# Kernel optimization log

Measured on AMD Instinct MI355X. Metric: run time of the kernel, lower is better.

The kernel has to match this reference:

```python
import jax, jax.numpy as jnp
import numpy as np

N_LAYERS = 3
N_HEADS = 8
N_HIDDEN = 16  # hidden_dim // n_heads
HIDDEN = 128
SLOPE = 0.2


def setup_inputs() -> dict:
    key = jax.random.key(0)
    ks = jax.random.split(key, 7)
    B, N, Din, Dh = 4, 512, 2, HIDDEN
    node_features = jax.random.normal(ks[0], (B, N, Din), dtype=jnp.float32)
    adj = jax.random.randint(ks[1], (B, N, N), 0, 2).astype(jnp.int32)
    adj = jnp.maximum(adj, jnp.eye(N, dtype=jnp.int32)[None])  # self loops -> no empty softmax rows
    s = 1.0 / np.sqrt(Dh)
    W_in = jax.random.normal(ks[2], (Din, Dh), dtype=jnp.float32) * (1.0 / np.sqrt(Din))
    W_l = jax.random.normal(ks[3], (N_LAYERS, Dh, N_HEADS * N_HIDDEN), dtype=jnp.float32) * s
    W_r = jax.random.normal(ks[4], (N_LAYERS, Dh, N_HEADS * N_HIDDEN), dtype=jnp.float32) * s
    attn_a = jax.random.normal(ks[5], (N_LAYERS, N_HIDDEN), dtype=jnp.float32) * (1.0 / np.sqrt(N_HIDDEN))
    W_out = jax.random.normal(ks[6], (Dh, 1), dtype=jnp.float32) * s
    return {"node_features": node_features, "adj": adj, "W_in": W_in,
            "W_l": W_l, "W_r": W_r, "attn_a": attn_a, "W_out": W_out}


def _gatv2_layer(h, adj, Wl, Wr, a):
    # h: [B,N,Dh]; adj: [B,N,N] int; Wl/Wr: [Dh, H*F]; a: [F]
    B, N, _ = h.shape
    g_l = (h @ Wl).reshape(B, N, N_HEADS, N_HIDDEN)
    g_r = (h @ Wr).reshape(B, N, N_HEADS, N_HIDDEN)
    # torch: g_sum[b,i,j] = g_l[b,j] + g_r[b,i]  (repeat vs repeat_interleave)
    g_sum = g_r[:, :, None, :, :] + g_l[:, None, :, :, :]  # [B,N,N,H,F]
    e = jnp.einsum('bijhf,f->bijh', jax.nn.leaky_relu(g_sum, SLOPE), a)  # [B,N,N,H]
    e = jnp.where(adj[..., None] == 0, -jnp.inf, e)
    att = jax.nn.softmax(e, axis=2)  # softmax over neighbors j
    out = jnp.einsum('bijh,bjhf->bihf', att, g_r)  # aggregate g_r (per source)
    return out.reshape(B, N, N_HEADS * N_HIDDEN)


def reference(node_features, adj, W_in, W_l, W_r, attn_a, W_out):
    h = node_features @ W_in  # [B,N,128]
    for i in range(N_LAYERS):
        h = _gatv2_layer(h, adj, W_l[i], W_r[i], attn_a[i])
    return h @ W_out  # [B,N,1]
```

## Files before the change

kernel.cpp:

```cpp
#include <hip/hip_runtime.h>
#include <cstdint>
#include <math.h>

#define NB 4
#define NN 512
#define DH 128
#define NHEADS 8
#define NHID 16
#define ITILE 64
#define SENTINEL -1e30f

__global__ __launch_bounds__(512, 1) void gat_layer(
    const int lay,
    const float* __restrict__ X, const float* __restrict__ hin,
    float* __restrict__ hout,
    const float* __restrict__ Win,
    const float* __restrict__ WlL, const float* __restrict__ WrL,
    const float* __restrict__ a_vec, const float* __restrict__ Wout,
    float* __restrict__ out, uint32_t* __restrict__ adjb,
    const int* __restrict__ adj)
{
    __shared__ __align__(16) float smem[23968];
    float* s_W   = smem;
    float* s_acc = smem + 4096;
    float* s_Win = smem + 20480;
    float* s_dgl = smem + 20736;
    float* s_dgr = smem + 21248;
    float* s_m   = smem + 21760;
    float* s_l   = smem + 22800;
    float* s_M   = smem + 23840;
    float* s_inv = smem + 23904;
    float4* Sgl  = (float4*)(smem + 4096);
    float4* Sgr  = (float4*)(smem + 12288);

    const int blk = blockIdx.x;
    const int it  = blk & 7;
    const int bh  = blk >> 3;
    const int b   = bh >> 3;
    const int hh  = bh & 7;
    const int i0  = it * ITILE;
    const int t   = threadIdx.x;
    const int il  = t & 31;
    const int js  = t >> 5;
    const int r0  = i0 + il;
    const int r1  = r0 + 32;

    {
        const int sk = t >> 2, sq = (t & 3) * 4;
        *(float4*)&s_W[sk * 32 + sq]      = *(const float4*)&WlL[sk * DH + hh * NHID + sq];
        *(float4*)&s_W[sk * 32 + 16 + sq] = *(const float4*)&WrL[sk * DH + hh * NHID + sq];
        if (lay == 0 && t < 64) ((float4*)s_Win)[t] = ((const float4*)Win)[t];
    }

    float a[16];
#pragma unroll
    for (int q = 0; q < 4; ++q) {
        const float4 v = ((const float4*)a_vec)[q];
        a[4*q+0] = v.x; a[4*q+1] = v.y; a[4*q+2] = v.z; a[4*q+3] = v.w;
    }

    uint32_t mask0, mask1;
    if (lay == 0) {
        const int4* p0 = (const int4*)(adj + ((size_t)(b * NN + r0)) * NN + js * 32);
        const int4* p1 = (const int4*)(adj + ((size_t)(b * NN + r1)) * NN + js * 32);
        uint32_t m0 = 0, m1 = 0;
#pragma unroll
        for (int c = 0; c < 8; ++c) {
            const int4 v0 = p0[c], v1 = p1[c];
            m0 |= (v0.x != 0 ? 1u : 0u) << (c * 4 + 0);
            m0 |= (v0.y != 0 ? 1u : 0u) << (c * 4 + 1);
            m0 |= (v0.z != 0 ? 1u : 0u) << (c * 4 + 2);
            m0 |= (v0.w != 0 ? 1u : 0u) << (c * 4 + 3);
            m1 |= (v1.x != 0 ? 1u : 0u) << (c * 4 + 0);
            m1 |= (v1.y != 0 ? 1u : 0u) << (c * 4 + 1);
            m1 |= (v1.z != 0 ? 1u : 0u) << (c * 4 + 2);
            m1 |= (v1.w != 0 ? 1u : 0u) << (c * 4 + 3);
        }
        mask0 = m0; mask1 = m1;
        adjb[((size_t)(b * NN + r0)) * 16 + js] = m0;
        adjb[((size_t)(b * NN + r1)) * 16 + js] = m1;
    } else {
        mask0 = adjb[((size_t)(b * NN + r0)) * 16 + js];
        mask1 = adjb[((size_t)(b * NN + r1)) * 16 + js];
    }
    __syncthreads();

    float4 agl[4], agr[4];
#pragma unroll
    for (int q = 0; q < 4; ++q) {
        agl[q].x = 0.f; agl[q].y = 0.f; agl[q].z = 0.f; agl[q].w = 0.f;
        agr[q].x = 0.f; agr[q].y = 0.f; agr[q].z = 0.f; agr[q].w = 0.f;
    }
    {
        const float* hrow = (lay > 0) ? (hin + ((size_t)(b * NN + t)) * DH) : nullptr;
        float x0 = 0.f, x1 = 0.f;
        if (lay == 0) {
            x0 = X[(b * NN + t) * 2 + 0];
            x1 = X[(b * NN + t) * 2 + 1];
        }
#pragma unroll 2
        for (int k = 0; k < DH; k += 4) {
            float4 h4;
            if (lay == 0) {
                const float4 w0 = *(const float4*)&s_Win[k];
                const float4 w1 = *(const float4*)&s_Win[DH + k];
                h4.x = x0 * w0.x + x1 * w1.x;
                h4.y = x0 * w0.y + x1 * w1.y;
                h4.z = x0 * w0.z + x1 * w1.z;
                h4.w = x0 * w0.w + x1 * w1.w;
            } else {
                h4 = *(const float4*)&hrow[k];
            }
            const float* hp = &h4.x;
#pragma unroll
            for (int kk = 0; kk < 4; ++kk) {
                const float hk = hp[kk];
                const float* wrow = &s_W[(k + kk) * 32];
#pragma unroll
                for (int q = 0; q < 4; ++q) {
                    const float4 wl = *(const float4*)&wrow[q * 4];
                    const float4 wr = *(const float4*)&wrow[16 + q * 4];
                    agl[q].x = fmaf(hk, wl.x, agl[q].x);
                    agl[q].y = fmaf(hk, wl.y, agl[q].y);
                    agl[q].z = fmaf(hk, wl.z, agl[q].z);
                    agl[q].w = fmaf(hk, wl.w, agl[q].w);
                    agr[q].x = fmaf(hk, wr.x, agr[q].x);
                    agr[q].y = fmaf(hk, wr.y, agr[q].y);
                    agr[q].z = fmaf(hk, wr.z, agr[q].z);
                    agr[q].w = fmaf(hk, wr.w, agr[q].w);
                }
            }
        }
    }
    {
        float dl = 0.f, dr = 0.f;
#pragma unroll
        for (int q = 0; q < 4; ++q) {
            dl = fmaf(a[4*q+0], agl[q].x, dl); dl = fmaf(a[4*q+1], agl[q].y, dl);
            dl = fmaf(a[4*q+2], agl[q].z, dl); dl = fmaf(a[4*q+3], agl[q].w, dl);
            dr = fmaf(a[4*q+0], agr[q].x, dr); dr = fmaf(a[4*q+1], agr[q].y, dr);
            dr = fmaf(a[4*q+2], agr[q].z, dr); dr = fmaf(a[4*q+3], agr[q].w, dr);
        }
        s_dgl[t] = dl;
        s_dgr[t] = dr;
    }
#pragma unroll
    for (int q = 0; q < 4; ++q) {
        Sgl[q * 512 + t] = agl[q];
        Sgr[q * 512 + t] = agr[q];
    }
    __syncthreads();

    float gri0[16], gri1[16];
#pragma unroll
    for (int q = 0; q < 4; ++q) {
        const float4 v0 = Sgr[q * 512 + r0];
        const float4 v1 = Sgr[q * 512 + r1];
        gri0[4*q+0] = v0.x; gri0[4*q+1] = v0.y; gri0[4*q+2] = v0.z; gri0[4*q+3] = v0.w;
        gri1[4*q+0] = v1.x; gri1[4*q+1] = v1.y; gri1[4*q+2] = v1.z; gri1[4*q+3] = v1.w;
    }

    const float c0 = 0.6f * s_dgr[r0];
    const float c1 = 0.6f * s_dgr[r1];
    const int jbase = js * 32;
    float sc0[32], sc1[32];
#pragma unroll
    for (int jj = 0; jj < 32; ++jj) {
        const int j = jbase + jj;
        const float dj = s_dgl[j];
        float s0 = 0.f, s1 = 0.f;
#pragma unroll
        for (int q = 0; q < 4; ++q) {
            const float4 g = Sgl[q * 512 + j];
            float v;
            v = g.x + gri0[4*q+0]; s0 = fmaf(a[4*q+0], fabsf(v), s0);
            v = g.y + gri0[4*q+1]; s0 = fmaf(a[4*q+1], fabsf(v), s0);
            v = g.z + gri0[4*q+2]; s0 = fmaf(a[4*q+2], fabsf(v), s0);
            v = g.w + gri0[4*q+3]; s0 = fmaf(a[4*q+3], fabsf(v), s0);
            v = g.x + gri1[4*q+0]; s1 = fmaf(a[4*q+0], fabsf(v), s1);
            v = g.y + gri1[4*q+1]; s1 = fmaf(a[4*q+1], fabsf(v), s1);
            v = g.z + gri1[4*q+2]; s1 = fmaf(a[4*q+2], fabsf(v), s1);
            v = g.w + gri1[4*q+3]; s1 = fmaf(a[4*q+3], fabsf(v), s1);
        }
        const float b0 = fmaf(0.6f, dj, c0);
        const float b1 = fmaf(0.6f, dj, c1);
        sc0[jj] = ((mask0 >> jj) & 1u) ? fmaf(0.4f, s0, b0) : SENTINEL;
        sc1[jj] = ((mask1 >> jj) & 1u) ? fmaf(0.4f, s1, b1) : SENTINEL;
    }

    float m0 = sc0[0], m1 = sc1[0];
#pragma unroll
    for (int jj = 1; jj < 32; ++jj) { m0 = fmaxf(m0, sc0[jj]); m1 = fmaxf(m1, sc1[jj]); }
    float l0 = 0.f, l1 = 0.f;
#pragma unroll
    for (int jj = 0; jj < 32; ++jj) {
        sc0[jj] = __expf(sc0[jj] - m0); l0 += sc0[jj];
        sc1[jj] = __expf(sc1[jj] - m1); l1 += sc1[jj];
    }
    s_m[js * 65 + il]      = m0;
    s_m[js * 65 + il + 32] = m1;
    s_l[js * 65 + il]      = l0;
    s_l[js * 65 + il + 32] = l1;

    float acc0[16], acc1[16];
#pragma unroll
    for (int f = 0; f < 16; ++f) { acc0[f] = 0.f; acc1[f] = 0.f; }
#pragma unroll
    for (int jj = 0; jj < 32; ++jj) {
        const int j = jbase + jj;
        const float p0 = sc0[jj], p1 = sc1[jj];
#pragma unroll
        for (int q = 0; q < 4; ++q) {
            const float4 g = Sgr[q * 512 + j];
            acc0[4*q+0] = fmaf(p0, g.x, acc0[4*q+0]);
            acc0[4*q+1] = fmaf(p0, g.y, acc0[4*q+1]);
            acc0[4*q+2] = fmaf(p0, g.z, acc0[4*q+2]);
            acc0[4*q+3] = fmaf(p0, g.w, acc0[4*q+3]);
            acc1[4*q+0] = fmaf(p1, g.x, acc1[4*q+0]);
            acc1[4*q+1] = fmaf(p1, g.y, acc1[4*q+1]);
            acc1[4*q+2] = fmaf(p1, g.z, acc1[4*q+2]);
            acc1[4*q+3] = fmaf(p1, g.w, acc1[4*q+3]);
        }
    }
    __syncthreads();

    if (t < 64) {
        float M = SENTINEL;
#pragma unroll
        for (int k = 0; k < 16; ++k) M = fmaxf(M, s_m[k * 65 + t]);
        float L = 0.f;
#pragma unroll
        for (int k = 0; k < 16; ++k) L += s_l[k * 65 + t] * __expf(s_m[k * 65 + t] - M);
        s_M[t]   = M;
        s_inv[t] = 1.f / L;
    }
    __syncthreads();

    {
        const float k0 = __expf(m0 - s_M[il])      * s_inv[il];
        const float k1 = __expf(m1 - s_M[il + 32]) * s_inv[il + 32];
        const int swz = il & 3;
        float* base_a = s_acc + js * 1024;
#pragma unroll
        for (int q = 0; q < 4; ++q) {
            float4 v0, v1;
            v0.x = acc0[4*q+0] * k0; v0.y = acc0[4*q+1] * k0;
            v0.z = acc0[4*q+2] * k0; v0.w = acc0[4*q+3] * k0;
            v1.x = acc1[4*q+0] * k1; v1.y = acc1[4*q+1] * k1;
            v1.z = acc1[4*q+2] * k1; v1.w = acc1[4*q+3] * k1;
            *(float4*)(base_a + il * 16        + 4 * (q ^ swz)) = v0;
            *(float4*)(base_a + (il + 32) * 16 + 4 * (q ^ swz)) = v1;
        }
    }
    __syncthreads();

    {
        const int i  = t >> 4;
        const int f  = t & 15;
        const int e  = f & 3, qf = f >> 2;
#pragma unroll
        for (int r = 0; r < 2; ++r) {
            const int lr = i + r * 32;
            const int w  = lr * 16 + 4 * (qf ^ (lr & 3)) + e;
            float o = 0.f;
#pragma unroll
            for (int k = 0; k < 16; ++k) o += s_acc[k * 1024 + w];
            const int grow = i0 + lr;
            if (Wout) {
                float v = o * Wout[hh * NHID + f];
#pragma unroll
                for (int off = 8; off; off >>= 1) v += __shfl_xor(v, off);
                if (f == 0) atomicAdd(out + b * NN + grow, v);
            } else {
                hout[((size_t)(b * NN + grow)) * DH + hh * NHID + f] = o;
            }
        }
    }

    if (lay == 1 && blk < 4) out[blk * 512 + t] = 0.f;
}

extern "C" void kernel_launch(void* const* d_in, const int* in_sizes, int n_in,
                              void* d_out, int out_size, void* d_ws, size_t ws_size,
                              hipStream_t stream) {
    const float* X    = (const float*)d_in[0];
    const int*   adj  = (const int*)  d_in[1];
    const float* Win  = (const float*)d_in[2];
    const float* Wl   = (const float*)d_in[3];
    const float* Wr   = (const float*)d_in[4];
    const float* Aa   = (const float*)d_in[5];
    const float* Wout = (const float*)d_in[6];
    float* out = (float*)d_out;

    float*    ws   = (float*)d_ws;
    float*    h_a  = ws;
    float*    h_b  = ws + 262144;
    uint32_t* adjb = (uint32_t*)(ws + 524288);

    gat_layer<<<256, 512, 0, stream>>>(0, X, nullptr, h_a, Win,
        Wl,              Wr,              Aa,      nullptr, out, adjb, adj);
    gat_layer<<<256, 512, 0, stream>>>(1, nullptr, h_a, h_b, Win,
        Wl + DH * DH,    Wr + DH * DH,    Aa + 16, nullptr, out, adjb, adj);
    gat_layer<<<256, 512, 0, stream>>>(2, nullptr, h_b, nullptr, Win,
        Wl + 2 * DH * DH, Wr + 2 * DH * DH, Aa + 32, Wout,  out, adjb, adj);
}
```

Before: 170.5 us.

## Restructure per-block projection to stage h tiles in LDS with scalar weight loads

The Wl/Wr projection is rewritten so the block stages 128-row tiles of h into padded shared memory. Each thread computes 8 output columns for one row, reading weights via wave-uniform scalar loads from global memory instead of an LDS weight copy. This aims to reduce register pressure and improve h load coalescing. In exchange it adds four tile iterations with extra barriers and a larger shared memory footprint.

```diff
diff --git a/kernel.cpp b/kernel.cpp
--- a/kernel.cpp
+++ b/kernel.cpp
@@ -20,18 +20,19 @@
     float* __restrict__ out, uint32_t* __restrict__ adjb,
     const int* __restrict__ adj)
 {
-    __shared__ __align__(16) float smem[23968];
-    float* s_W   = smem;
-    float* s_acc = smem + 4096;
-    float* s_Win = smem + 20480;
-    float* s_dgl = smem + 20736;
-    float* s_dgr = smem + 21248;
-    float* s_m   = smem + 21760;
-    float* s_l   = smem + 22800;
-    float* s_M   = smem + 23840;
-    float* s_inv = smem + 23904;
-    float4* Sgl  = (float4*)(smem + 4096);
-    float4* Sgr  = (float4*)(smem + 12288);
+    __shared__ __align__(16) float smem[36512];
+    float* s_h   = smem;
+    float* s_acc = smem;
+    float* Sgl_f = smem + 16896;
+    float* Sgr_f = smem + 25088;
+    float* s_dgl = smem + 33280;
+    float* s_dgr = smem + 33792;
+    float* s_m   = smem + 34304;
+    float* s_l   = smem + 35344;
+    float* s_M   = smem + 36384;
+    float* s_inv = smem + 36448;
+    float4* Sgl  = (float4*)Sgl_f;
+    float4* Sgr  = (float4*)Sgr_f;
 
     const int blk = blockIdx.x;
     const int it  = blk & 7;
@@ -45,13 +46,6 @@
     const int r0  = i0 + il;
     const int r1  = r0 + 32;
 
-    {
-        const int sk = t >> 2, sq = (t & 3) * 4;
-        *(float4*)&s_W[sk * 32 + sq]      = *(const float4*)&WlL[sk * DH + hh * NHID + sq];
-        *(float4*)&s_W[sk * 32 + 16 + sq] = *(const float4*)&WrL[sk * DH + hh * NHID + sq];
-        if (lay == 0 && t < 64) ((float4*)s_Win)[t] = ((const float4*)Win)[t];
-    }
-
     float a[16];
 #pragma unroll
     for (int q = 0; q < 4; ++q) {
@@ -83,71 +77,72 @@
         mask0 = adjb[((size_t)(b * NN + r0)) * 16 + js];
         mask1 = adjb[((size_t)(b * NN + r1)) * 16 + js];
     }
-    __syncthreads();
-
-    float4 agl[4], agr[4];
-#pragma unroll
-    for (int q = 0; q < 4; ++q) {
-        agl[q].x = 0.f; agl[q].y = 0.f; agl[q].z = 0.f; agl[q].w = 0.f;
-        agr[q].x = 0.f; agr[q].y = 0.f; agr[q].z = 0.f; agr[q].w = 0.f;
-    }
-    {
-        const float* hrow = (lay > 0) ? (hin + ((size_t)(b * NN + t)) * DH) : nullptr;
-        float x0 = 0.f, x1 = 0.f;
-        if (lay == 0) {
-            x0 = X[(b * NN + t) * 2 + 0];
-            x1 = X[(b * NN + t) * 2 + 1];
-        }
-#pragma unroll 2
-        for (int k = 0; k < DH; k += 4) {
+
+    const int coct = __builtin_amdgcn_readfirstlane(t >> 7);
+    const int rg   = t & 127;
+    const float* Wbase = ((coct < 2) ? WlL : WrL) + hh * NHID + (coct & 1) * 8;
+
+#pragma unroll 1
+    for (int qt = 0; qt < 4; ++qt) {
+        const int rbase = qt * 128;
+        __syncthreads();
+        for (int i = t; i < 128 * 32; i += 512) {
+            const int row = i >> 5, q = i & 31;
             float4 h4;
             if (lay == 0) {
-                const float4 w0 = *(const float4*)&s_Win[k];
-                const float4 w1 = *(const float4*)&s_Win[DH + k];
+                const float x0 = X[(b * NN + rbase + row) * 2 + 0];
+                const float x1 = X[(b * NN + rbase + row) * 2 + 1];
+                const float4 w0 = *(const float4*)&Win[q * 4];
+                const float4 w1 = *(const float4*)&Win[DH + q * 4];
                 h4.x = x0 * w0.x + x1 * w1.x;
                 h4.y = x0 * w0.y + x1 * w1.y;
                 h4.z = x0 * w0.z + x1 * w1.z;
                 h4.w = x0 * w0.w + x1 * w1.w;
             } else {
-                h4 = *(const float4*)&hrow[k];
+                h4 = *(const float4*)&hin[((size_t)(b * NN + rbase + row)) * DH + q * 4];
             }
-            const float* hp = &h4.x;
+            *(float4*)&s_h[row * 132 + q * 4] = h4;
+        }
+        __syncthreads();
+        float acc[8] = {};
+#pragma unroll 2
+        for (int k = 0; k < DH; k += 4) {
+            const float4 hv = *(const float4*)&s_h[rg * 132 + k];
+            const float* hp = &hv.x;
 #pragma unroll
             for (int kk = 0; kk < 4; ++kk) {
                 const float hk = hp[kk];
-                const float* wrow = &s_W[(k + kk) * 32];
-#pragma unroll
-                for (int q = 0; q < 4; ++q) {
-                    const float4 wl = *(const float4*)&wrow[q * 4];
-                    const float4 wr = *(const float4*)&wrow[16 + q * 4];
-                    agl[q].x = fmaf(hk, wl.x, agl[q].x);
-                    agl[q].y = fmaf(hk, wl.y, agl[q].y);
-                    agl[q].z = fmaf(hk, wl.z, agl[q].z);
-                    agl[q].w = fmaf(hk, wl.w, agl[q].w);
-                    agr[q].x = fmaf(hk, wr.x, agr[q].x);
-                    agr[q].y = fmaf(hk, wr.y, agr[q].y);
-                    agr[q].z = fmaf(hk, wr.z, agr[q].z);
-                    agr[q].w = fmaf(hk, wr.w, agr[q].w);
-                }
+                const float* wr = Wbase + (k + kk) * DH;
+#pragma unroll
+                for (int c = 0; c < 8; ++c)
+                    acc[c] = fmaf(hk, wr[c], acc[c]);
             }
         }
-    }
+        {
+            float4 v0, v1;
+            v0.x = acc[0]; v0.y = acc[1]; v0.z = acc[2]; v0.w = acc[3];
+            v1.x = acc[4]; v1.y = acc[5]; v1.z = acc[6]; v1.w = acc[7];
+            float4* Sg = (coct < 2) ? Sgl : Sgr;
+            const int q0 = (coct & 1) * 2;
+            Sg[q0 * 512       + rbase + rg] = v0;
+            Sg[(q0 + 1) * 512 + rbase + rg] = v1;
+        }
+    }
+    __syncthreads();
+
     {
         float dl = 0.f, dr = 0.f;
 #pragma unroll
         for (int q = 0; q < 4; ++q) {
-            dl = fmaf(a[4*q+0], agl[q].x, dl); dl = fmaf(a[4*q+1], agl[q].y, dl);
-            dl = fmaf(a[4*q+2], agl[q].z, dl); dl = fmaf(a[4*q+3], agl[q].w, dl);
-            dr = fmaf(a[4*q+0], agr[q].x, dr); dr = fmaf(a[4*q+1], agr[q].y, dr);
-            dr = fmaf(a[4*q+2], agr[q].z, dr); dr = fmaf(a[4*q+3], agr[q].w, dr);
+            const float4 vl = Sgl[q * 512 + t];
+            const float4 vr = Sgr[q * 512 + t];
+            dl = fmaf(a[4*q+0], vl.x, dl); dl = fmaf(a[4*q+1], vl.y, dl);
+            dl = fmaf(a[4*q+2], vl.z, dl); dl = fmaf(a[4*q+3], vl.w, dl);
+            dr = fmaf(a[4*q+0], vr.x, dr); dr = fmaf(a[4*q+1], vr.y, dr);
+            dr = fmaf(a[4*q+2], vr.z, dr); dr = fmaf(a[4*q+3], vr.w, dr);
         }
         s_dgl[t] = dl;
         s_dgr[t] = dr;
-    }
-#pragma unroll
-    for (int q = 0; q < 4; ++q) {
-        Sgl[q * 512 + t] = agl[q];
-        Sgr[q * 512 + t] = agr[q];
     }
     __syncthreads();
 
@@ -298,9 +293,9 @@
     uint32_t* adjb = (uint32_t*)(ws + 524288);
 
     gat_layer<<<256, 512, 0, stream>>>(0, X, nullptr, h_a, Win,
-        Wl,              Wr,              Aa,      nullptr, out, adjb, adj);
+        Wl,               Wr,               Aa,      nullptr, out, adjb, adj);
     gat_layer<<<256, 512, 0, stream>>>(1, nullptr, h_a, h_b, Win,
-        Wl + DH * DH,    Wr + DH * DH,    Aa + 16, nullptr, out, adjb, adj);
+        Wl + DH * DH,     Wr + DH * DH,     Aa + 16, nullptr, out, adjb, adj);
     gat_layer<<<256, 512, 0, stream>>>(2, nullptr, h_b, nullptr, Win,
-        Wl + 2 * DH * DH, Wr + 2 * DH * DH, Aa + 32, Wout,  out, adjb, adj);
+        Wl + 2 * DH * DH, Wr + 2 * DH * DH, Aa + 32, Wout,    out, adjb, adj);
 }
```

Measured after the change: 222.3 us. 1.3x slower.
